# Kernel optimization log

Hardware: AMD Instinct MI355X
Metric: run time of the kernel (lower is better)

Reference implementation:

```python
import jax, jax.numpy as jnp
import numpy as np

# 4D convolution via lax.conv_general_dilated with 4 spatial dims.
# Layout: input (N, C, D, H, W, T), kernel (O, I, d, h, w, t).
DN = ('NCDHWT', 'OIDHWT', 'NCDHWT')


def conv4d(x, w, b, pad):
    # torch Conv2d/Conv4d is cross-correlation, matching lax.conv_general_dilated
    y = jax.lax.conv_general_dilated(
        x, w, window_strides=(1, 1, 1, 1),
        padding=[(pad, pad)] * 4, dimension_numbers=DN)
    return y + b.reshape(1, -1, 1, 1, 1, 1)


def _kaiming(key, shape):
    fan_out = shape[0] * int(np.prod(shape[2:]))
    std = np.sqrt(2.0 / fan_out)
    return (jax.random.normal(key, shape, dtype=jnp.float32) * std).astype(jnp.float32)


def setup_inputs() -> dict:
    key = jax.random.key(0)
    ks = jax.random.split(key, 11)
    B, W, H = 256, 16, 16
    corr = jax.random.normal(ks[0], (B, W * H, W, H), dtype=jnp.float32)
    w1 = _kaiming(ks[1], (1, 1, 17, 17, 9, 9))
    w2 = _kaiming(ks[2], (1, 1, 7, 7, 7, 7))
    w3 = _kaiming(ks[3], (1, 1, 5, 5, 5, 5))
    w4 = _kaiming(ks[4], (1, 1, 3, 3, 3, 3))
    w5 = _kaiming(ks[5], (1, 1, 8, 8, 1, 1))
    b1 = jax.random.normal(ks[6], (1,), dtype=jnp.float32) * 0.01
    b2 = jax.random.normal(ks[7], (1,), dtype=jnp.float32) * 0.01
    b3 = jax.random.normal(ks[8], (1,), dtype=jnp.float32) * 0.01
    b4 = jax.random.normal(ks[9], (1,), dtype=jnp.float32) * 0.01
    b5 = jax.random.normal(ks[10], (1,), dtype=jnp.float32) * 0.01
    return {"corr": corr, "w1": w1, "b1": b1, "w2": w2, "b2": b2,
            "w3": w3, "b3": b3, "w4": w4, "b4": b4, "w5": w5, "b5": b5}


def reference(corr, w1, b1, w2, b2, w3, b3, w4, b4, w5, b5):
    B, HW, W, H = corr.shape
    x = corr.reshape(B, 1, W, H, W, H)          # (B,1,16,16,16,16)
    x = jax.nn.relu(conv4d(x, w1, b1, 4))       # (B,1, 8, 8,16,16)
    x = jax.nn.relu(conv4d(x, w2, b2, 3))
    x = jax.nn.relu(conv4d(x, w3, b3, 2))
    x = jax.nn.relu(conv4d(x, w4, b4, 1))
    out = jax.nn.sigmoid(conv4d(x, w5, b5, 0))  # (B,1, 1, 1,16,16)
    return out.reshape(B, 1, W, H)
```

## Files before the change

kernel.cpp:

```cpp
#include <hip/hip_runtime.h>
#include <math.h>


typedef short bf16x8 __attribute__((ext_vector_type(8)));
typedef float f32x4 __attribute__((ext_vector_type(4)));
typedef unsigned int u32x4 __attribute__((ext_vector_type(4)));

#define XTS 64
#define NROWS 396
#define ZROW 384
#define TTS 72

__device__ __forceinline__ int xts(int row, int col) {
  return row * XTS + (col ^ ((row & 7) << 3));
}

__device__ __forceinline__ unsigned short f2bf(float f) {
  unsigned int u = __float_as_uint(f);
  u += 0x7fffu + ((u >> 16) & 1u);
  return (unsigned short)(u >> 16);
}

template <int KSZ, int PAD>
__device__ __forceinline__ void build_mid(const float* __restrict__ w,
                                          unsigned short* __restrict__ Bg, int gid) {
  const int lane = gid & 63;
  const int n_tile = (gid >> 6) & 3;
  const int chunk = (gid >> 8) & 1;
  const int tap = gid >> 9;
  const int kw = tap / KSZ, kt = tap - kw * KSZ;
  const int dh_o = n_tile * 16 + (lane & 15);
  const int d_o = dh_o >> 3, h_o = dh_o & 7;
  const int kbase = chunk * 32 + (lane >> 4) * 8;
  unsigned int pk[4];
#pragma unroll
  for (int p = 0; p < 4; ++p) {
    unsigned short half[2];
#pragma unroll
    for (int s = 0; s < 2; ++s) {
      const int k = kbase + p * 2 + s;
      const int d_i = k >> 3, h_i = k & 7;
      const int kd = d_i - d_o + PAD, kh = h_i - h_o + PAD;
      float v = 0.f;
      if (kd >= 0 && kd < KSZ && kh >= 0 && kh < KSZ)
        v = w[((kd * KSZ + kh) * KSZ + kw) * KSZ + kt];
      half[s] = f2bf(v);
    }
    pk[p] = (unsigned int)half[0] | ((unsigned int)half[1] << 16);
  }
  *(int4*)(Bg + (size_t)gid * 8) = make_int4(pk[0], pk[1], pk[2], pk[3]);
}

__global__ __launch_bounds__(256) void build_all(const float* __restrict__ w1,
                                                 const float* __restrict__ w2,
                                                 const float* __restrict__ w3,
                                                 const float* __restrict__ w4,
                                                 unsigned short* __restrict__ Bg1,
                                                 unsigned short* __restrict__ Bg2,
                                                 unsigned short* __restrict__ Bg3,
                                                 unsigned short* __restrict__ Bg4) {
  const int bid = blockIdx.x, tid = threadIdx.x;
  if (bid < 648) {
    const int gid = bid * 256 + tid;
    const int lane = gid & 63;
    const int n_tile = (gid >> 6) & 3;
    const int chunk = (gid >> 8) & 7;
    const int kwkt = gid >> 11;
    const int kw = kwkt / 9, kt = kwkt - kw * 9;
    const int dh_o = n_tile * 16 + (lane & 15);
    const int d_o = dh_o >> 3, h_o = dh_o & 7;
    const int kbase = chunk * 32 + (lane >> 4) * 8;
    unsigned int pk[4];
#pragma unroll
    for (int p = 0; p < 4; ++p) {
      unsigned short half[2];
#pragma unroll
      for (int s = 0; s < 2; ++s) {
        const int k = kbase + p * 2 + s;
        const int d_i = k >> 4, h_i = k & 15;
        const int kd = d_i - d_o + 4, kh = h_i - h_o + 4;
        float v = 0.f;
        if (kd >= 0 && kd < 17 && kh >= 0 && kh < 17)
          v = w1[((kd * 17 + kh) * 9 + kw) * 9 + kt];
        half[s] = f2bf(v);
      }
      pk[p] = (unsigned int)half[0] | ((unsigned int)half[1] << 16);
    }
    *(int4*)(Bg1 + (size_t)gid * 8) = make_int4(pk[0], pk[1], pk[2], pk[3]);
  } else if (bid < 746) {
    build_mid<7, 3>(w2, Bg2, (bid - 648) * 256 + tid);
  } else if (bid < 796) {
    build_mid<5, 2>(w3, Bg3, (bid - 746) * 256 + tid);
  } else {
    build_mid<3, 1>(w4, Bg4, (bid - 796) * 256 + tid);
  }
}

__device__ __forceinline__ void l1_loadA(const unsigned short* XT, const int (&arb)[4],
                                         int kt, int tl, int quad, int chalf,
                                         bf16x8 (&A)[4]) {
  const int sw = ((tl + kt) & 7) << 3;
  const int c = (quad * 8 + chalf * 32) ^ sw;
  const int ko = kt * XTS;
#pragma unroll
  for (int m = 0; m < 4; ++m)
    A[m] = *(const bf16x8*)&XT[arb[m] + ko + c];
}

__device__ __forceinline__ void l1_loadB(const unsigned short* __restrict__ Bt, int kt,
                                         bf16x8 (&B)[8]) {
#pragma unroll
  for (int c = 0; c < 2; ++c)
#pragma unroll
    for (int n = 0; n < 4; ++n)
      B[c * 4 + n] = *(const bf16x8*)(Bt + (size_t)kt * 16384 + c * 2048 + n * 512);
}

__device__ __forceinline__ void mfma_half(const bf16x8 (&A)[4], const bf16x8* B,
                                          f32x4 (&acc)[4][4]) {
  __builtin_amdgcn_s_setprio(1);
#pragma unroll
  for (int m = 0; m < 4; ++m)
#pragma unroll
    for (int n = 0; n < 4; ++n)
      acc[m][n] = __builtin_amdgcn_mfma_f32_16x16x32_bf16(A[m], B[n], acc[m][n], 0, 0, 0);
  __builtin_amdgcn_s_setprio(0);
}

__global__ __launch_bounds__(256) void conv_l1_mfma(const float* __restrict__ x,
                                                    const unsigned short* __restrict__ Bg,
                                                    float* __restrict__ P) {
  __shared__ __align__(16) unsigned short XT[NROWS * XTS];
  const int bx = blockIdx.x;
  const int b = bx >> 1, khalf = bx & 1;
  const int tid = threadIdx.x;
  const int lane = tid & 63, wave = tid >> 6;
  const int quad = lane >> 4, tl = lane & 15;
  const float* xb = x + (size_t)b * 65536;
  f32x4 acc[4][4] = {};

  for (int j = tid; j < (NROWS * XTS) / 8; j += 256)
    *(int4*)&XT[j * 8] = make_int4(0, 0, 0, 0);
  __syncthreads();

  for (int qq = 0; qq < 2; ++qq) {
    const int q = khalf * 2 + qq;
    if (qq) __syncthreads();
#pragma unroll
    for (int it = 0; it < 8; ++it) {
      const int i = tid + it * 256;
      const int dhp = i >> 6, wtq = i & 63;
      const int r0 = (wtq >> 2) * 24 + (wtq & 3) * 4 + 4;
      const float4 ra = *(const float4*)(xb + (size_t)(q * 64 + 2 * dhp) * 256 + wtq * 4);
      const float4 rb =
          *(const float4*)(xb + (size_t)(q * 64 + 2 * dhp + 1) * 256 + wtq * 4);
      const float a0[4] = {ra.x, ra.y, ra.z, ra.w};
      const float a1[4] = {rb.x, rb.y, rb.z, rb.w};
#pragma unroll
      for (int j = 0; j < 4; ++j) {
        const unsigned int p = (unsigned int)f2bf(a0[j]) | ((unsigned int)f2bf(a1[j]) << 16);
        *(unsigned int*)&XT[xts(r0 + j, dhp * 2)] = p;
      }
    }
    __syncthreads();

    const unsigned short* Bt = Bg + (size_t)(q * 2) * 2048 + lane * 8;
    for (int kw = 0; kw < 9; ++kw) {
      int arb[4];
#pragma unroll
      for (int m = 0; m < 4; ++m) {
        const int w_i = wave * 4 + m + kw - 4;
        arb[m] = (((unsigned)w_i < 16u) ? (w_i * 24 + tl) : ZROW) * XTS;
      }
      bf16x8 B0[8], B1[8];
      l1_loadB(Bt, 0, B0);
#pragma unroll
      for (int kt = 0; kt < 9; ++kt) {
        bf16x8* Bc = (kt & 1) ? B1 : B0;
        bf16x8* Bn = (kt & 1) ? B0 : B1;
        if (kt < 8) l1_loadB(Bt, kt + 1, *(bf16x8(*)[8])Bn);
        bf16x8 A[4];
        l1_loadA(XT, arb, kt, tl, quad, 0, A);
        mfma_half(A, Bc, acc);
        l1_loadA(XT, arb, kt, tl, quad, 1, A);
        mfma_half(A, Bc + 4, acc);
      }
      Bt += 9 * 16384;
    }
  }

  float* Pb = P + (size_t)(khalf * 256 + b) * 16384;
#pragma unroll
  for (int m = 0; m < 4; ++m)
#pragma unroll
    for (int n = 0; n < 4; ++n) {
      const int dh_o = n * 16 + tl;
      const int wt0 = wave * 64 + m * 16 + quad * 4;
      *(float4*)&Pb[(size_t)dh_o * 256 + wt0] = *(const float4*)&acc[m][n];
    }
}

template <int KSZ, int PAD>
__device__ __forceinline__ void tail_load_tap(const unsigned short* XT,
                                              const unsigned short* __restrict__ Bg, int kwkt,
                                              int mw, int nh, int lane, int quad, int tl,
                                              bf16x8 (&A)[8], bf16x8 (&B)[4]) {
  const int kw = kwkt / KSZ, kt = kwkt - kw * KSZ;
  const int t_i = tl + kt - PAD;
  const bool tv = (unsigned)t_i < 16u;
  int ro[4];
#pragma unroll
  for (int m = 0; m < 4; ++m) {
    const int w_i = mw * 4 + m + kw - PAD;
    const bool v = tv && ((unsigned)w_i < 16u);
    const int row = v ? (w_i * 16 + t_i) : 256;
    ro[m] = row * TTS + quad * 8;
  }
#pragma unroll
  for (int c = 0; c < 2; ++c)
#pragma unroll
    for (int m = 0; m < 4; ++m)
      A[c * 4 + m] = *(const bf16x8*)&XT[ro[m] + c * 32];
#pragma unroll
  for (int c = 0; c < 2; ++c)
#pragma unroll
    for (int n = 0; n < 2; ++n)
      B[c * 2 + n] =
          *(const bf16x8*)(Bg + (((size_t)(kwkt * 2 + c) * 4 + (nh * 2 + n)) << 9) + lane * 8);
}

__device__ __forceinline__ void mfma8(const bf16x8 (&A)[8], const bf16x8 (&B)[4],
                                      f32x4 (&acc)[4][2]) {
  __builtin_amdgcn_s_setprio(1);
#pragma unroll
  for (int c = 0; c < 2; ++c)
#pragma unroll
    for (int m = 0; m < 4; ++m)
#pragma unroll
      for (int n = 0; n < 2; ++n)
        acc[m][n] = __builtin_amdgcn_mfma_f32_16x16x32_bf16(A[c * 4 + m], B[c * 2 + n],
                                                            acc[m][n], 0, 0, 0);
  __builtin_amdgcn_s_setprio(0);
}

template <int KSZ, int PAD, int NT>
__device__ __forceinline__ void run_layer(unsigned short* XT,
                                          const unsigned short* __restrict__ Bg,
                                          const float bias, int mw, int nh, int lane,
                                          int quad, int tl) {
  f32x4 acc[4][2] = {};
  {
    bf16x8 A0[8], B0[4], A1[8], B1[4];
    tail_load_tap<KSZ, PAD>(XT, Bg, 0, mw, nh, lane, quad, tl, A0, B0);
    int k = 0;
    while (true) {
      if (k + 1 < NT) tail_load_tap<KSZ, PAD>(XT, Bg, k + 1, mw, nh, lane, quad, tl, A1, B1);
      mfma8(A0, B0, acc);
      if (++k >= NT) break;
      if (k + 1 < NT) tail_load_tap<KSZ, PAD>(XT, Bg, k + 1, mw, nh, lane, quad, tl, A0, B0);
      mfma8(A1, B1, acc);
      if (++k >= NT) break;
    }
  }
  __syncthreads();
#pragma unroll
  for (int m = 0; m < 4; ++m)
#pragma unroll
    for (int n = 0; n < 2; ++n) {
      const int col = (nh * 2 + n) * 16 + tl;
      const int wt0 = mw * 64 + m * 16 + quad * 4;
#pragma unroll
      for (int j = 0; j < 4; ++j)
        XT[(wt0 + j) * TTS + col] = f2bf(fmaxf(acc[m][n][j] + bias, 0.f));
    }
  __syncthreads();
}

__global__ __launch_bounds__(512) void tail_fused(const float* __restrict__ P,
                                                  const unsigned short* __restrict__ Bg2,
                                                  const unsigned short* __restrict__ Bg3,
                                                  const unsigned short* __restrict__ Bg4,
                                                  const float* __restrict__ b1,
                                                  const float* __restrict__ b2,
                                                  const float* __restrict__ b3,
                                                  const float* __restrict__ b4,
                                                  const float* __restrict__ w5,
                                                  const float* __restrict__ b5,
                                                  float* __restrict__ out) {
  __shared__ __align__(16) unsigned short XT[257 * TTS];
  const int b = blockIdx.x;
  const int tid = threadIdx.x;
  const int lane = tid & 63, wave = tid >> 6;
  const int quad = lane >> 4, tl = lane & 15;
  const int mw = wave >> 1, nh = wave & 1;
  const float* p0 = P + (size_t)b * 16384;
  const float* p1 = p0 + (size_t)256 * 16384;
  const float bias1 = b1[0];

  if (tid < 9) *(int4*)&XT[256 * TTS + tid * 8] = make_int4(0, 0, 0, 0);
#pragma unroll
  for (int it = 0; it < 4; ++it) {
    const int i = tid + it * 512;
    const int dhp = i >> 6, wtq = i & 63;
    const size_t off0 = (size_t)(2 * dhp) * 256 + wtq * 4;
    const float4 r0a = *(const float4*)(p0 + off0);
    const float4 r0b = *(const float4*)(p1 + off0);
    const float4 r1a = *(const float4*)(p0 + off0 + 256);
    const float4 r1b = *(const float4*)(p1 + off0 + 256);
    float a0[4] = {r0a.x + r0b.x, r0a.y + r0b.y, r0a.z + r0b.z, r0a.w + r0b.w};
    float a1[4] = {r1a.x + r1b.x, r1a.y + r1b.y, r1a.z + r1b.z, r1a.w + r1b.w};
#pragma unroll
    for (int j = 0; j < 4; ++j) {
      const unsigned short lo = f2bf(fmaxf(a0[j] + bias1, 0.f));
      const unsigned short hi = f2bf(fmaxf(a1[j] + bias1, 0.f));
      const unsigned int p = (unsigned int)lo | ((unsigned int)hi << 16);
      *(unsigned int*)&XT[(wtq * 4 + j) * TTS + dhp * 2] = p;
    }
  }
  __syncthreads();

  run_layer<7, 3, 49>(XT, Bg2, b2[0], mw, nh, lane, quad, tl);
  run_layer<5, 2, 25>(XT, Bg3, b3[0], mw, nh, lane, quad, tl);
  run_layer<3, 1, 9>(XT, Bg4, b4[0], mw, nh, lane, quad, tl);

  if (tid < 256) {
    const int wt = tid;
    float s = b5[0];
    const unsigned short* row = &XT[wt * TTS];
#pragma unroll
    for (int k8 = 0; k8 < 8; ++k8) {
      const u32x4 v = *(const u32x4*)&row[k8 * 8];
      const unsigned int uu[4] = {(unsigned int)v.x, (unsigned int)v.y, (unsigned int)v.z,
                                  (unsigned int)v.w};
#pragma unroll
      for (int p = 0; p < 4; ++p) {
        const float lo = __uint_as_float(uu[p] << 16);
        const float hi = __uint_as_float(uu[p] & 0xFFFF0000u);
        s += lo * w5[k8 * 8 + p * 2] + hi * w5[k8 * 8 + p * 2 + 1];
      }
    }
    out[(size_t)b * 256 + wt] = 1.f / (1.f + expf(-s));
  }
}

extern "C" void kernel_launch(void* const* d_in, const int* in_sizes, int n_in,
                              void* d_out, int out_size, void* d_ws, size_t ws_size,
                              hipStream_t stream) {
  const float* corr = (const float*)d_in[0];
  const float* w1 = (const float*)d_in[1];
  const float* b1 = (const float*)d_in[2];
  const float* w2 = (const float*)d_in[3];
  const float* b2 = (const float*)d_in[4];
  const float* w3 = (const float*)d_in[5];
  const float* b3 = (const float*)d_in[6];
  const float* w4 = (const float*)d_in[7];
  const float* b4 = (const float*)d_in[8];
  const float* w5 = (const float*)d_in[9];
  const float* b5 = (const float*)d_in[10];

  float* P = (float*)d_ws;
  unsigned short* Bg1 = (unsigned short*)((char*)d_ws + (64u << 20));
  unsigned short* Bg2 = Bg1 + (size_t)81 * 8 * 4 * 64 * 8;
  unsigned short* Bg3 = Bg2 + (size_t)49 * 2 * 4 * 64 * 8;
  unsigned short* Bg4 = Bg3 + (size_t)25 * 2 * 4 * 64 * 8;

  build_all<<<814, 256, 0, stream>>>(w1, w2, w3, w4, Bg1, Bg2, Bg3, Bg4);
  conv_l1_mfma<<<512, 256, 0, stream>>>(corr, Bg1, P);
  tail_fused<<<256, 512, 0, stream>>>(P, Bg2, Bg3, Bg4, b1, b2, b3, b4, w5, b5,
                                      (float*)d_out);
}
```

Measured before the change: 266.2 us.

## Reuse LDS A-fragments across kw taps with sliding window in tail layers

Restructures the tail conv layers so the outer loop runs over kt and the inner loop over kw. A four-entry rotating register window of A fragments is kept, so each kw step loads only one new row from LDS instead of four. B weight fragments stay double-buffered from global memory. This is meant to cut LDS read traffic in the MFMA loops of layers 2-4, at the cost of full unrolling and more register pressure.

```diff
diff --git a/kernel.cpp b/kernel.cpp
--- a/kernel.cpp
+++ b/kernel.cpp
@@ -201,65 +201,61 @@
 }
 
 template <int KSZ, int PAD>
-__device__ __forceinline__ void tail_load_tap(const unsigned short* XT,
-                                              const unsigned short* __restrict__ Bg, int kwkt,
-                                              int mw, int nh, int lane, int quad, int tl,
-                                              bf16x8 (&A)[8], bf16x8 (&B)[4]) {
-  const int kw = kwkt / KSZ, kt = kwkt - kw * KSZ;
-  const int t_i = tl + kt - PAD;
-  const bool tv = (unsigned)t_i < 16u;
-  int ro[4];
-#pragma unroll
-  for (int m = 0; m < 4; ++m) {
-    const int w_i = mw * 4 + m + kw - PAD;
-    const bool v = tv && ((unsigned)w_i < 16u);
-    const int row = v ? (w_i * 16 + t_i) : 256;
-    ro[m] = row * TTS + quad * 8;
-  }
-#pragma unroll
-  for (int c = 0; c < 2; ++c)
-#pragma unroll
-    for (int m = 0; m < 4; ++m)
-      A[c * 4 + m] = *(const bf16x8*)&XT[ro[m] + c * 32];
-#pragma unroll
-  for (int c = 0; c < 2; ++c)
-#pragma unroll
-    for (int n = 0; n < 2; ++n)
-      B[c * 2 + n] =
-          *(const bf16x8*)(Bg + (((size_t)(kwkt * 2 + c) * 4 + (nh * 2 + n)) << 9) + lane * 8);
-}
-
-__device__ __forceinline__ void mfma8(const bf16x8 (&A)[8], const bf16x8 (&B)[4],
-                                      f32x4 (&acc)[4][2]) {
-  __builtin_amdgcn_s_setprio(1);
-#pragma unroll
-  for (int c = 0; c < 2; ++c)
-#pragma unroll
-    for (int m = 0; m < 4; ++m)
-#pragma unroll
-      for (int n = 0; n < 2; ++n)
-        acc[m][n] = __builtin_amdgcn_mfma_f32_16x16x32_bf16(A[c * 4 + m], B[c * 2 + n],
-                                                            acc[m][n], 0, 0, 0);
-  __builtin_amdgcn_s_setprio(0);
-}
-
-template <int KSZ, int PAD, int NT>
 __device__ __forceinline__ void run_layer(unsigned short* XT,
                                           const unsigned short* __restrict__ Bg,
                                           const float bias, int mw, int nh, int lane,
                                           int quad, int tl) {
   f32x4 acc[4][2] = {};
-  {
-    bf16x8 A0[8], B0[4], A1[8], B1[4];
-    tail_load_tap<KSZ, PAD>(XT, Bg, 0, mw, nh, lane, quad, tl, A0, B0);
-    int k = 0;
-    while (true) {
-      if (k + 1 < NT) tail_load_tap<KSZ, PAD>(XT, Bg, k + 1, mw, nh, lane, quad, tl, A1, B1);
-      mfma8(A0, B0, acc);
-      if (++k >= NT) break;
-      if (k + 1 < NT) tail_load_tap<KSZ, PAD>(XT, Bg, k + 1, mw, nh, lane, quad, tl, A0, B0);
-      mfma8(A1, B1, acc);
-      if (++k >= NT) break;
+  const unsigned short* BgL = Bg + lane * 8;
+#pragma unroll
+  for (int kt = 0; kt < KSZ; ++kt) {
+    const int t_i = tl + kt - PAD;
+    const bool tv = (unsigned)t_i < 16u;
+    bf16x8 Aw[2][4];
+#pragma unroll
+    for (int m = 0; m < 4; ++m) {
+      const int w_i = mw * 4 + m - PAD;
+      const int row = (tv && (unsigned)w_i < 16u) ? (w_i * 16 + t_i) : 256;
+      const int ro = row * TTS + quad * 8;
+      Aw[0][m] = *(const bf16x8*)&XT[ro];
+      Aw[1][m] = *(const bf16x8*)&XT[ro + 32];
+    }
+    bf16x8 Bb[2][4];
+#pragma unroll
+    for (int c = 0; c < 2; ++c)
+#pragma unroll
+      for (int n = 0; n < 2; ++n)
+        Bb[0][c * 2 + n] =
+            *(const bf16x8*)(BgL + (((size_t)(kt * 2 + c) * 4 + (nh * 2 + n)) << 9));
+#pragma unroll
+    for (int kw = 0; kw < KSZ; ++kw) {
+      const int cur = kw & 1, nxt = cur ^ 1;
+      if (kw + 1 < KSZ) {
+        const int kwkt = (kw + 1) * KSZ + kt;
+#pragma unroll
+        for (int c = 0; c < 2; ++c)
+#pragma unroll
+          for (int n = 0; n < 2; ++n)
+            Bb[nxt][c * 2 + n] =
+                *(const bf16x8*)(BgL + (((size_t)(kwkt * 2 + c) * 4 + (nh * 2 + n)) << 9));
+      }
+      __builtin_amdgcn_s_setprio(1);
+#pragma unroll
+      for (int c = 0; c < 2; ++c)
+#pragma unroll
+        for (int m = 0; m < 4; ++m)
+#pragma unroll
+          for (int n = 0; n < 2; ++n)
+            acc[m][n] = __builtin_amdgcn_mfma_f32_16x16x32_bf16(
+                Aw[c][(kw + m) & 3], Bb[cur][c * 2 + n], acc[m][n], 0, 0, 0);
+      __builtin_amdgcn_s_setprio(0);
+      if (kw + 1 < KSZ) {
+        const int w_i = mw * 4 + 4 + kw - PAD;
+        const int row = (tv && (unsigned)w_i < 16u) ? (w_i * 16 + t_i) : 256;
+        const int ro = row * TTS + quad * 8;
+        Aw[0][kw & 3] = *(const bf16x8*)&XT[ro];
+        Aw[1][kw & 3] = *(const bf16x8*)&XT[ro + 32];
+      }
     }
   }
   __syncthreads();
@@ -319,9 +315,9 @@
   }
   __syncthreads();
 
-  run_layer<7, 3, 49>(XT, Bg2, b2[0], mw, nh, lane, quad, tl);
-  run_layer<5, 2, 25>(XT, Bg3, b3[0], mw, nh, lane, quad, tl);
-  run_layer<3, 1, 9>(XT, Bg4, b4[0], mw, nh, lane, quad, tl);
+  run_layer<7, 3>(XT, Bg2, b2[0], mw, nh, lane, quad, tl);
+  run_layer<5, 2>(XT, Bg3, b3[0], mw, nh, lane, quad, tl);
+  run_layer<3, 1>(XT, Bg4, b4[0], mw, nh, lane, quad, tl);
 
   if (tid < 256) {
     const int wt = tid;
```

Result: faster. 257.7 us (-3.2%).
